# Kernel tuning notes

Measured on AMD Instinct MI355X. Metric: run time of the kernel, lower is better.

## Reference

```python
import jax, jax.numpy as jnp
import numpy as np
from jax import lax

B, DIM, H, W = 8, 128, 64, 64
CQ, DI, DS, RK = 32, 64, 16, 2  # quarter dim, d_inner=2*CQ, d_state, dt_rank=ceil(32/16)
EPS = 1e-5


def _dw(x, w, dil):
    # depthwise conv, x: [B,C,H,W], w: [C,1,kh,kw], torch padding='same'
    return lax.conv_general_dilated(x, w, (1, 1), 'SAME', rhs_dilation=(dil, dil),
                                    dimension_numbers=('NCHW', 'OIHW', 'NCHW'),
                                    feature_group_count=x.shape[1])


def _ln(x, g, b):
    mu = jnp.mean(x, -1, keepdims=True)
    v = jnp.mean((x - mu) ** 2, -1, keepdims=True)
    return (x - mu) * lax.rsqrt(v + EPS) * g + b


def _bn_eval(x, g, b):
    # BatchNorm2d eval mode with default running stats (mean 0, var 1)
    return x * lax.rsqrt(jnp.float32(1.0) + EPS) * g[None, :, None, None] + b[None, :, None, None]


def _axial_dw(x, kh, kw, k3, g, b, dil):
    y = _dw(x, kw, dil)   # (1,w) mixer
    y = _dw(y, kh, dil)   # (h,1) mixer
    y = _dw(y, k3, dil)   # 3x3 dw
    return _bn_eval(y, g, b) + x


def _vss(x, ln_g, ln_b, in_w, conv_w, conv_b, xproj_w, dtw, dtb, A_logs, Ds, on_g, on_b, out_w):
    # x: [B,H,W,CQ] channels-last; VMamba VSSBlock: x + SS2D(LN(x))
    Bb, Hh, Ww, _ = x.shape
    L = Hh * Ww
    xz = _ln(x, ln_g, ln_b) @ in_w.T                      # [B,H,W,2*DI]
    xw, z = jnp.split(xz, 2, axis=-1)
    xc = jax.nn.silu(_dw(xw.transpose(0, 3, 1, 2), conv_w, 1) + conv_b[None, :, None, None])
    xf = xc.reshape(Bb, DI, L)                            # row-major scan
    xwh = xc.transpose(0, 1, 3, 2).reshape(Bb, DI, L)     # column-major scan
    xs = jnp.stack([xf, xwh, jnp.flip(xf, -1), jnp.flip(xwh, -1)], axis=1)  # [B,4,DI,L]
    x_dbl = jnp.einsum('bkdl,kcd->bkcl', xs, xproj_w)     # [B,4,RK+2*DS,L]
    delta = jax.nn.softplus(jnp.einsum('bkrl,kdr->bkdl', x_dbl[:, :, :RK], dtw) + dtb[None, :, :, None])
    Bs, Cs = x_dbl[:, :, RK:RK + DS], x_dbl[:, :, RK + DS:]
    A = -jnp.exp(A_logs)                                  # [4,DI,DS]

    def step(h, t):
        u, d, Bt, Ct = t                                  # u,d:[B,4,DI]; Bt,Ct:[B,4,DS]
        h = h * jnp.exp(d[..., None] * A) + (d * u)[..., None] * Bt[:, :, None, :]
        return h, jnp.einsum('bkdn,bkn->bkd', h, Ct)

    seq = (xs.transpose(3, 0, 1, 2), delta.transpose(3, 0, 1, 2),
           Bs.transpose(3, 0, 1, 2), Cs.transpose(3, 0, 1, 2))
    _, ys = lax.scan(step, jnp.zeros((Bb, 4, DI, DS), x.dtype), seq)  # [L,B,4,DI]
    ys = ys.transpose(1, 2, 3, 0) + Ds[None, :, :, None] * xs         # [B,4,DI,L]
    y = ys[:, 0] + jnp.flip(ys[:, 2], -1)
    y_wh = ys[:, 1] + jnp.flip(ys[:, 3], -1)
    y = y + y_wh.reshape(Bb, DI, Ww, Hh).transpose(0, 1, 3, 2).reshape(Bb, DI, L)
    y = _ln(y.reshape(Bb, DI, Hh, Ww).transpose(0, 2, 3, 1), on_g, on_b)
    return x + (y * jax.nn.silu(z)) @ out_w.T


def _forward(x, dw1_kh, dw1_kw, dw1_k3, dw1_g, dw1_b, dw2_kh, dw2_kw, dw2_k3, dw2_g, dw2_b,
             dw3_kh, dw3_kw, dw3_k3, dw3_g, dw3_b, ln_g, ln_b, in_w, conv_w, conv_b, xproj_w,
             dtw, dtb, A_logs, Ds, on_g, on_b, out_w, scale1, scale2, scale3, scale4, bn_g, bn_b):
    x1, x2, x3, x4 = jnp.split(x, 4, axis=1)
    vp = (ln_g, ln_b, in_w, conv_w, conv_b, xproj_w, dtw, dtb, A_logs, Ds, on_g, on_b, out_w)

    def branch(xi, kh, kw, k3, g, b, dil, s):
        y = _axial_dw(xi, kh, kw, k3, g, b, dil)
        y = _vss(y.transpose(0, 2, 3, 1), *vp).transpose(0, 3, 1, 2)
        return y * s

    y1 = branch(x1, dw1_kh, dw1_kw, dw1_k3, dw1_g, dw1_b, 1, scale1)
    y2 = branch(x2, dw2_kh, dw2_kw, dw2_k3, dw2_g, dw2_b, 2, scale2)
    y3 = branch(x3, dw3_kh, dw3_kw, dw3_k3, dw3_g, dw3_b, 3, scale3)
    y4 = x4 * scale4
    return jax.nn.relu(_bn_eval(jnp.concatenate([y1, y2, y3, y4], 1), bn_g, bn_b))


def setup_inputs():
    ks = jax.random.split(jax.random.key(0), 40)
    rn = lambda k, s, sc: jax.random.normal(k, s, jnp.float32) * sc
    inp = {'x': jax.random.normal(ks[0], (B, DIM, H, W), jnp.float32)}
    for i, n in enumerate(['dw1', 'dw2', 'dw3']):
        inp[n + '_kh'] = rn(ks[1 + 3 * i], (CQ, 1, 7, 1), 0.2)
        inp[n + '_kw'] = rn(ks[2 + 3 * i], (CQ, 1, 1, 7), 0.2)
        inp[n + '_k3'] = rn(ks[3 + 3 * i], (CQ, 1, 3, 3), 0.2)
        inp[n + '_g'] = jnp.ones((CQ,))
        inp[n + '_b'] = jnp.zeros((CQ,))
    inp['ln_g'] = jnp.ones((CQ,))
    inp['ln_b'] = jnp.zeros((CQ,))
    inp['in_w'] = rn(ks[10], (2 * DI, CQ), 0.1)
    inp['conv_w'] = rn(ks[11], (DI, 1, 3, 3), 0.2)
    inp['conv_b'] = jnp.zeros((DI,))
    inp['xproj_w'] = rn(ks[12], (4, RK + 2 * DS, DI), 0.1)
    inp['dtw'] = rn(ks[13], (4, DI, RK), 0.5)
    inp['dtb'] = rn(ks[14], (4, DI), 0.5)
    inp['A_logs'] = jnp.log(jnp.broadcast_to(jnp.arange(1, DS + 1, dtype=jnp.float32), (4, DI, DS)))
    inp['Ds'] = jnp.ones((4, DI))
    inp['on_g'] = jnp.ones((DI,))
    inp['on_b'] = jnp.zeros((DI,))
    inp['out_w'] = rn(ks[15], (CQ, DI), 0.1)
    for n in ['scale1', 'scale2', 'scale3', 'scale4']:
        inp[n] = jnp.ones((1,))
    inp['bn_g'] = jnp.ones((DIM,))
    inp['bn_b'] = jnp.zeros((DIM,))
    return inp


def reference(x, dw1_kh, dw1_kw, dw1_k3, dw1_g, dw1_b, dw2_kh, dw2_kw, dw2_k3, dw2_g, dw2_b,
              dw3_kh, dw3_kw, dw3_k3, dw3_g, dw3_b, ln_g, ln_b, in_w, conv_w, conv_b, xproj_w,
              dtw, dtb, A_logs, Ds, on_g, on_b, out_w, scale1, scale2, scale3, scale4, bn_g, bn_b):
    return _forward(x, dw1_kh, dw1_kw, dw1_k3, dw1_g, dw1_b, dw2_kh, dw2_kw, dw2_k3, dw2_g, dw2_b,
                    dw3_kh, dw3_kw, dw3_k3, dw3_g, dw3_b, ln_g, ln_b, in_w, conv_w, conv_b, xproj_w,
                    dtw, dtb, A_logs, Ds, on_g, on_b, out_w, scale1, scale2, scale3, scale4, bn_g, bn_b)
```

## Files before the change

kernel.cpp:

```cpp
#include <hip/hip_runtime.h>
#include <hip/hip_bf16.h>
#include <cstdint>

typedef unsigned short ushort_t;
typedef float f32x2 __attribute__((ext_vector_type(2)));

__device__ __forceinline__ float softplus2(float x){
    return fmaxf(x, 0.f) + __logf(1.f + __expf(-fabsf(x)));
}
__device__ __forceinline__ float siluf(float x){
    return x / (1.f + __expf(-x));
}
__device__ __forceinline__ float b2f(ushort_t u){
    union { uint32_t i; float f; } v; v.i = ((uint32_t)u)<<16; return v.f;
}
__device__ __forceinline__ ushort_t f2b(float f){
    uint32_t x = __float_as_uint(f);
    uint32_t r = (x + 0x7FFFu + ((x>>16)&1u)) >> 16;
    return (ushort_t)r;
}

struct AxialParams {
    const float* kh[3]; const float* kw[3]; const float* k3[3];
    const float* g[3];  const float* b[3];
};

__global__ __launch_bounds__(256) void k_axial(const float* __restrict__ x,
                                               float* __restrict__ Y0, AxialParams P){
    __shared__ float s0[4096];
    __shared__ float s1[4096];
    int bid = blockIdx.x;
    int i = bid >> 8;
    int rem = bid & 255;
    int b = rem >> 5, c = rem & 31;
    int dil = i + 1;
    const float* xin = x + ((size_t)(b*128 + i*32 + c))*4096;
    float wkw[7], wkh[7], wk3[9];
    #pragma unroll
    for(int t=0;t<7;t++){ wkw[t]=P.kw[i][c*7+t]; wkh[t]=P.kh[i][c*7+t]; }
    #pragma unroll
    for(int t=0;t<9;t++) wk3[t]=P.k3[i][c*9+t];
    float gc = P.g[i][c], bc = P.b[i][c];
    int tid = threadIdx.x;
    for(int idx=tid; idx<4096; idx+=256) s0[idx]=xin[idx];
    __syncthreads();
    for(int idx=tid; idx<4096; idx+=256){
        int h=idx>>6, w=idx&63; float a=0.f;
        #pragma unroll
        for(int t=0;t<7;t++){ int ww=w+(t-3)*dil; if(ww>=0&&ww<64) a=fmaf(s0[h*64+ww],wkw[t],a); }
        s1[idx]=a;
    }
    __syncthreads();
    for(int idx=tid; idx<4096; idx+=256){
        int h=idx>>6, w=idx&63; float a=0.f;
        #pragma unroll
        for(int t=0;t<7;t++){ int hh=h+(t-3)*dil; if(hh>=0&&hh<64) a=fmaf(s1[hh*64+w],wkh[t],a); }
        s0[idx]=a;
    }
    __syncthreads();
    const float inv = rsqrtf(1.00001f);
    float* out = Y0 + ((size_t)(i*8+b)*32 + c)*4096;
    for(int idx=tid; idx<4096; idx+=256){
        int h=idx>>6, w=idx&63; float a=0.f;
        #pragma unroll
        for(int t=0;t<9;t++){
            int hh=h+((t/3)-1)*dil, ww=w+((t%3)-1)*dil;
            if(hh>=0&&hh<64&&ww>=0&&ww<64) a=fmaf(s0[hh*64+ww],wk3[t],a);
        }
        out[idx] = a*inv*gc + bc + xin[idx];
    }
}

__global__ __launch_bounds__(256) void k_lnproj(const float* __restrict__ Y0,
        const float* __restrict__ ln_g, const float* __restrict__ ln_b,
        const float* __restrict__ in_w, ushort_t* __restrict__ XW, ushort_t* __restrict__ ZS){
    __shared__ float W[128*32];
    int tid=threadIdx.x;
    for(int idx=tid; idx<4096; idx+=256) W[idx]=in_w[idx];
    __syncthreads();
    int pg = blockIdx.x*256 + tid;
    int ib = pg>>12, p = pg&4095;
    const float* src = Y0 + (size_t)ib*32*4096;
    float t[32];
    float mu=0.f;
    #pragma unroll
    for(int c=0;c<32;c++){ t[c]=src[c*4096+p]; mu+=t[c]; }
    mu *= (1.f/32.f);
    float v=0.f;
    #pragma unroll
    for(int c=0;c<32;c++){ float d=t[c]-mu; v+=d*d; }
    v *= (1.f/32.f);
    float rs = rsqrtf(v+1e-5f);
    #pragma unroll
    for(int c=0;c<32;c++) t[c] = (t[c]-mu)*rs*ln_g[c] + ln_b[c];
    ushort_t* xw = XW + (size_t)ib*64*4096 + p;
    ushort_t* zs = ZS + (size_t)ib*64*4096 + p;
    for(int j=0;j<64;j++){
        float a=0.f, a2=0.f;
        #pragma unroll
        for(int c=0;c<32;c++){
            a  = fmaf(t[c], W[j*32+c],      a);
            a2 = fmaf(t[c], W[(j+64)*32+c], a2);
        }
        xw[(size_t)j*4096] = f2b(a);
        zs[(size_t)j*4096] = f2b(siluf(a2));
    }
}

__global__ __launch_bounds__(256) void k_dwt(const ushort_t* __restrict__ XW,
        const float* __restrict__ cw, const float* __restrict__ cb,
        ushort_t* __restrict__ XC, ushort_t* __restrict__ XCT){
    __shared__ ushort_t sin_[4096];
    __shared__ ushort_t tr[64*66];
    int bid=blockIdx.x, tid=threadIdx.x;
    int d = bid&63;
    const ushort_t* src = XW + (size_t)bid*4096;
    for(int idx=tid; idx<1024; idx+=256)
        *reinterpret_cast<ushort4*>(&sin_[idx*4]) = *reinterpret_cast<const ushort4*>(&src[idx*4]);
    float wk[9];
    #pragma unroll
    for(int t=0;t<9;t++) wk[t]=cw[d*9+t];
    float bias=cb[d];
    __syncthreads();
    ushort_t* outp = XC + (size_t)bid*4096;
    for(int idx=tid; idx<4096; idx+=256){
        int h=idx>>6, wq=idx&63;
        float a=bias;
        #pragma unroll
        for(int t=0;t<9;t++){
            int hh=h+(t/3)-1, ww=wq+(t%3)-1;
            if(hh>=0&&hh<64&&ww>=0&&ww<64) a=fmaf(b2f(sin_[hh*64+ww]),wk[t],a);
        }
        ushort_t vb = f2b(siluf(a));
        outp[idx]=vb;
        tr[wq*66+h]=vb;
    }
    __syncthreads();
    ushort_t* outt = XCT + (size_t)bid*4096;
    for(int idx=tid; idx<4096; idx+=256){
        outt[idx]=tr[(idx>>6)*66+(idx&63)];
    }
}

__global__ __launch_bounds__(256) void k_transpose(const ushort_t* __restrict__ src, ushort_t* __restrict__ dst){
    __shared__ ushort_t tile[64*66];
    size_t plane = blockIdx.x;
    const ushort_t* s = src + plane*4096;
    ushort_t* d = dst + plane*4096;
    int tid=threadIdx.x;
    for(int idx=tid; idx<4096; idx+=256){
        int h=idx>>6, w=idx&63;
        tile[w*66+h]=s[idx];
    }
    __syncthreads();
    for(int idx=tid; idx<4096; idx+=256){
        d[idx]=tile[(idx>>6)*66 + (idx&63)];
    }
}

__global__ __launch_bounds__(256) void k_xdbl(const ushort_t* __restrict__ XC, const ushort_t* __restrict__ XCT,
        const float* __restrict__ xproj, ushort_t* __restrict__ XBb, ushort_t* __restrict__ XCc,
        float* __restrict__ DT){
    __shared__ float Wt[64][36];
    int bid=blockIdx.x; int tid=threadIdx.x;
    int ibk = bid>>4; int lb = bid&15;
    int k = ibk & 3; int ib = ibk>>2;
    for(int idx=tid; idx<2176; idx+=256){
        int c=idx>>6, dd=idx&63;
        Wt[dd][c]=xproj[k*2176+idx];
    }
    __syncthreads();
    int l = lb*256+tid;
    const ushort_t* src = ((k&1)?XCT:XC) + (size_t)ib*64*4096;
    int idxl = (k&2)? (4095-l) : l;
    float acc[34];
    #pragma unroll
    for(int c=0;c<34;c++) acc[c]=0.f;
    for(int dd=0;dd<64;dd++){
        float u = b2f(src[(size_t)dd*4096 + idxl]);
        float wv[36];
        const float4* wp = reinterpret_cast<const float4*>(&Wt[dd][0]);
        *reinterpret_cast<float4*>(&wv[0])  = wp[0];
        *reinterpret_cast<float4*>(&wv[4])  = wp[1];
        *reinterpret_cast<float4*>(&wv[8])  = wp[2];
        *reinterpret_cast<float4*>(&wv[12]) = wp[3];
        *reinterpret_cast<float4*>(&wv[16]) = wp[4];
        *reinterpret_cast<float4*>(&wv[20]) = wp[5];
        *reinterpret_cast<float4*>(&wv[24]) = wp[6];
        *reinterpret_cast<float4*>(&wv[28]) = wp[7];
        *reinterpret_cast<float2*>(&wv[32]) = *reinterpret_cast<const float2*>(&Wt[dd][32]);
        #pragma unroll
        for(int c=0;c<34;c++) acc[c] = fmaf(u, wv[c], acc[c]);
    }
    DT[((size_t)ibk*2)*4096 + l]   = acc[0];
    DT[((size_t)ibk*2+1)*4096 + l] = acc[1];
    ushort_t* ob = XBb + ((size_t)ibk*16)*4096 + l;
    ushort_t* oc = XCc + ((size_t)ibk*16)*4096 + l;
    #pragma unroll
    for(int c=0;c<16;c++){
        ob[(size_t)c*4096]=f2b(acc[2+c]);
        oc[(size_t)c*4096]=f2b(acc[18+c]);
    }
}


template<bool UNI>
__device__ __forceinline__ void scan1_body(int w,int d,float dt0,float dt1,float db,
    const float* An, f32x2* h2, float& S,
    const float (*sB)[64][16], const float (*sdt)[64][2], const ushort_t (*su)[66])
{
    for(int s=0;s<64;s++){
        const float* dp=&sdt[w][s][0];
        float delta=softplus2(fmaf(dt0,dp[0],fmaf(dt1,dp[1],db)));
        S+=delta;
        int j = w? 63-s : s;
        float du = delta*b2f(su[j][d]);
        float bb[16];
        const float4* bp=reinterpret_cast<const float4*>(&sB[w][s][0]);
        reinterpret_cast<float4*>(bb)[0]=bp[0];
        reinterpret_cast<float4*>(bb)[1]=bp[1];
        reinterpret_cast<float4*>(bb)[2]=bp[2];
        reinterpret_cast<float4*>(bb)[3]=bp[3];
        if(UNI){
            float r1=__expf(delta*An[0]);
            f32x2 a={r1,r1*r1}, rq={r1*r1,r1*r1}, du2={du,du};
            const f32x2* b2p=reinterpret_cast<const f32x2*>(bb);
            #pragma unroll
            for(int i=0;i<8;i++){ h2[i]=h2[i]*a+du2*b2p[i]; a=a*rq; }
        } else {
            float* hf=reinterpret_cast<float*>(h2);
            #pragma unroll
            for(int n=0;n<16;n++){ float a=__expf(delta*An[n]); hf[n]=fmaf(hf[n],a,du*bb[n]); }
        }
    }
}

__global__ __launch_bounds__(128) void k_scan1(const ushort_t* __restrict__ XBb, const float* __restrict__ DT,
        const ushort_t* __restrict__ XC, const ushort_t* __restrict__ XCT,
        const float* __restrict__ dtw, const float* __restrict__ dtb,
        const float* __restrict__ A_logs,
        ushort_t* __restrict__ CHS, float* __restrict__ SD){
    __shared__ float sB[2][64][16];
    __shared__ float sdt[2][64][2];
    __shared__ ushort_t su[64][66];
    int bid=blockIdx.x, tid=threadIdx.x;
    int ib = bid>>7; int rem = bid&127; int p = rem>>6; int ch = rem&63;
    int w = tid>>6, d = tid&63;
    int l0 = ch*64, r0 = 4032 - l0;
    const ushort_t* B0 = XBb + (size_t)(4*ib+p)*16*4096;
    const ushort_t* B1 = XBb + (size_t)(4*ib+p+2)*16*4096;
    for(int idx=tid; idx<512; idx+=128){
        int w2=idx>>8, n=(idx>>4)&15, q=(idx&15)*4;
        const ushort_t* Bs = w2? B1 : B0;
        int base = (w2? r0 : l0) + q;
        ushort4 v = *reinterpret_cast<const ushort4*>(&Bs[(size_t)n*4096 + base]);
        sB[w2][q+0][n]=b2f(v.x); sB[w2][q+1][n]=b2f(v.y); sB[w2][q+2][n]=b2f(v.z); sB[w2][q+3][n]=b2f(v.w);
    }
    {
        const float* D0 = DT + (size_t)(4*ib+p)*2*4096;
        const float* D1 = DT + (size_t)(4*ib+p+2)*2*4096;
        int r=tid>>6, s=tid&63;
        sdt[0][s][r] = D0[(size_t)r*4096 + l0 + s];
        sdt[1][s][r] = D1[(size_t)r*4096 + r0 + s];
    }
    const ushort_t* U = (p?XCT:XC) + (size_t)ib*64*4096;
    for(int idx=tid; idx<1024; idx+=128){
        int r=idx>>4, q=(idx&15)*4;
        ushort4 v = *reinterpret_cast<const ushort4*>(&U[(size_t)r*4096 + l0 + q]);
        su[q+0][r]=v.x; su[q+1][r]=v.y; su[q+2][r]=v.z; su[q+3][r]=v.w;
    }
    __syncthreads();
    int k = p + 2*w;
    float dt0=dtw[(k*64+d)*2], dt1=dtw[(k*64+d)*2+1], db=dtb[k*64+d];
    float An[16];
    #pragma unroll
    for(int n=0;n<16;n++) An[n] = -__expf(A_logs[(k*64+d)*16+n]);
    bool st = true;
    #pragma unroll
    for(int n=1;n<16;n++) st = st && (fabsf(An[n]-(n+1)*An[0]) <= 1e-4f*fabsf(An[n]) + 1e-6f);
    bool uni = (bool)__all((int)st);
    f32x2 h2[8];
    #pragma unroll
    for(int i=0;i<8;i++){ h2[i].x=0.f; h2[i].y=0.f; }
    float S=0.f;
    if(uni) scan1_body<true >(w,d,dt0,dt1,db,An,h2,S,sB,sdt,su);
    else    scan1_body<false>(w,d,dt0,dt1,db,An,h2,S,sB,sdt,su);
    int chd = w ? 63-ch : ch;
    ushort_t* o = CHS + ((size_t)(4*ib+k)*64 + chd)*1024 + d*16;
    const float* hf = reinterpret_cast<const float*>(h2);
    #pragma unroll
    for(int n=0;n<16;n++) o[n]=f2b(hf[n]);
    SD[((size_t)(4*ib+k)*64 + chd)*64 + d]=S;
}

__global__ __launch_bounds__(1024) void k_scan2(const float* __restrict__ A_logs,
        const float* __restrict__ SD, ushort_t* __restrict__ CHS){
    __shared__ float sS[4096];
    int ibk=blockIdx.x; int tid=threadIdx.x;
    for(int idx=tid; idx<4096; idx+=1024) sS[idx]=SD[(size_t)ibk*4096+idx];
    __syncthreads();
    int d=tid>>4, n=tid&15, k=ibk&3;
    float An = -__expf(A_logs[(k*64+d)*16+n]);
    float H=0.f;
    for(int c=0;c<64;c++){
        float pc = __expf(An*sS[c*64+d]);
        size_t o = ((size_t)ibk*64+c)*1024 + tid;
        float loc = b2f(CHS[o]);
        CHS[o]=f2b(H);
        H = fmaf(H, pc, loc);
    }
}

__device__ __forceinline__ const ushort_t* seg_src(int idx, int seg,
        const ushort_t* B0, const ushort_t* B1, const ushort_t* C0, const ushort_t* C1,
        int l0, int r0){
    int arr=idx>>8, w2=(idx>>7)&1, n=(idx>>3)&15, qi=idx&7;
    const ushort_t* S = arr? (w2?C1:C0) : (w2?B1:B0);
    int base = (w2? r0 : l0) + seg*32 + qi*4;
    return &S[(size_t)n*4096 + base];
}
__device__ __forceinline__ void seg_wr(int idx, ushort4 v,
        float (*sB)[32][16], float (*sC)[32][16]){
    int arr=idx>>8, w2=(idx>>7)&1, n=(idx>>3)&15, qi=idx&7;
    float (*dst)[32][16] = arr? sC : sB;
    int sl=qi*4;
    dst[w2][sl+0][n]=b2f(v.x); dst[w2][sl+1][n]=b2f(v.y);
    dst[w2][sl+2][n]=b2f(v.z); dst[w2][sl+3][n]=b2f(v.w);
}

template<bool UNI, int SEG>
__device__ __forceinline__ void scan3_seg(int w,int d,float dt0,float dt1,float db,
    const float* An, f32x2* h2,
    const float (*sB)[32][16], const float (*sC)[32][16],
    const float (*sdt)[64][2], const ushort_t (*su)[66], ushort_t (*sy)[66])
{
    for(int t=0;t<32;t++){
        int s = SEG*32 + t;
        const float* dp=&sdt[w][s][0];
        float delta=softplus2(fmaf(dt0,dp[0],fmaf(dt1,dp[1],db)));
        int j = w? 63-s : s;
        float du = delta*b2f(su[j][d]);
        float bb[16], cc[16];
        const float4* bp=reinterpret_cast<const float4*>(&sB[w][t][0]);
        const float4* cp=reinterpret_cast<const float4*>(&sC[w][t][0]);
        reinterpret_cast<float4*>(bb)[0]=bp[0]; reinterpret_cast<float4*>(bb)[1]=bp[1];
        reinterpret_cast<float4*>(bb)[2]=bp[2]; reinterpret_cast<float4*>(bb)[3]=bp[3];
        reinterpret_cast<float4*>(cc)[0]=cp[0]; reinterpret_cast<float4*>(cc)[1]=cp[1];
        reinterpret_cast<float4*>(cc)[2]=cp[2]; reinterpret_cast<float4*>(cc)[3]=cp[3];
        float y;
        if(UNI){
            float r1=__expf(delta*An[0]);
            f32x2 a={r1,r1*r1}, rq={r1*r1,r1*r1}, du2={du,du};
            f32x2 y2={0.f,0.f};
            const f32x2* b2p=reinterpret_cast<const f32x2*>(bb);
            const f32x2* c2p=reinterpret_cast<const f32x2*>(cc);
            #pragma unroll
            for(int i=0;i<8;i++){
                h2[i]=h2[i]*a+du2*b2p[i];
                y2=y2+h2[i]*c2p[i];
                a=a*rq;
            }
            y = y2.x + y2.y;
        } else {
            y=0.f;
            float* hf=reinterpret_cast<float*>(h2);
            #pragma unroll
            for(int n=0;n<16;n++){
                float a=__expf(delta*An[n]);
                hf[n]=fmaf(hf[n],a,du*bb[n]);
                y=fmaf(hf[n],cc[n],y);
            }
        }
        if(SEG==0) sy[j][d]=f2b(y);
        else       sy[j][d]=f2b(b2f(sy[j][d])+y);
    }
}

__global__ __launch_bounds__(128) void k_scan3(const ushort_t* __restrict__ XBb, const ushort_t* __restrict__ XCc,
        const float* __restrict__ DT,
        const ushort_t* __restrict__ XC, const ushort_t* __restrict__ XCT,
        const float* __restrict__ dtw, const float* __restrict__ dtb,
        const float* __restrict__ A_logs,
        const ushort_t* __restrict__ CHS,
        ushort_t* __restrict__ Y1, ushort_t* __restrict__ Y2){
    __shared__ float sB[2][32][16];
    __shared__ float sC[2][32][16];
    __shared__ float sdt[2][64][2];
    __shared__ ushort_t su[64][66];
    __shared__ ushort_t sy[64][66];
    int bid=blockIdx.x, tid=threadIdx.x;
    int ib = bid>>7; int rem = bid&127; int p = rem>>6; int ch = rem&63;
    int w = tid>>6, d = tid&63;
    int l0 = ch*64, r0 = 4032 - l0;
    const ushort_t* B0 = XBb + (size_t)(4*ib+p)*16*4096;
    const ushort_t* B1 = XBb + (size_t)(4*ib+p+2)*16*4096;
    const ushort_t* C0 = XCc + (size_t)(4*ib+p)*16*4096;
    const ushort_t* C1 = XCc + (size_t)(4*ib+p+2)*16*4096;
    for(int idx=tid; idx<512; idx+=128)
        seg_wr(idx, *reinterpret_cast<const ushort4*>(seg_src(idx,0,B0,B1,C0,C1,l0,r0)), sB, sC);
    {
        const float* D0 = DT + (size_t)(4*ib+p)*2*4096;
        const float* D1 = DT + (size_t)(4*ib+p+2)*2*4096;
        int r=tid>>6, s=tid&63;
        sdt[0][s][r] = D0[(size_t)r*4096 + l0 + s];
        sdt[1][s][r] = D1[(size_t)r*4096 + r0 + s];
    }
    const ushort_t* U = (p?XCT:XC) + (size_t)ib*64*4096;
    for(int idx=tid; idx<1024; idx+=128){
        int r=idx>>4, q=(idx&15)*4;
        ushort4 v = *reinterpret_cast<const ushort4*>(&U[(size_t)r*4096 + l0 + q]);
        su[q+0][r]=v.x; su[q+1][r]=v.y; su[q+2][r]=v.z; su[q+3][r]=v.w;
    }
    __syncthreads();
    ushort4 pf[4];
    #pragma unroll
    for(int r=0;r<4;r++)
        pf[r] = *reinterpret_cast<const ushort4*>(seg_src(tid+r*128,1,B0,B1,C0,C1,l0,r0));
    int k = p + 2*w;
    float dt0=dtw[(k*64+d)*2], dt1=dtw[(k*64+d)*2+1], db=dtb[k*64+d];
    float An[16];
    #pragma unroll
    for(int n=0;n<16;n++) An[n] = -__expf(A_logs[(k*64+d)*16+n]);
    bool st = true;
    #pragma unroll
    for(int n=1;n<16;n++) st = st && (fabsf(An[n]-(n+1)*An[0]) <= 1e-4f*fabsf(An[n]) + 1e-6f);
    bool uni = (bool)__all((int)st);
    int chd = w ? 63-ch : ch;
    const ushort_t* e = CHS + ((size_t)(4*ib+k)*64 + chd)*1024 + d*16;
    f32x2 h2[8];
    {
        float* hf = reinterpret_cast<float*>(h2);
        #pragma unroll
        for(int n=0;n<16;n++) hf[n]=b2f(e[n]);
    }
    if(uni) scan3_seg<true ,0>(w,d,dt0,dt1,db,An,h2,sB,sC,sdt,su,sy);
    else    scan3_seg<false,0>(w,d,dt0,dt1,db,An,h2,sB,sC,sdt,su,sy);
    __syncthreads();
    #pragma unroll
    for(int r=0;r<4;r++) seg_wr(tid+r*128, pf[r], sB, sC);
    __syncthreads();
    if(uni) scan3_seg<true ,1>(w,d,dt0,dt1,db,An,h2,sB,sC,sdt,su,sy);
    else    scan3_seg<false,1>(w,d,dt0,dt1,db,An,h2,sB,sC,sdt,su,sy);
    __syncthreads();
    ushort_t* Yb = (p?Y2:Y1) + (size_t)ib*64*4096;
    for(int idx=tid; idx<1024; idx+=128){
        int r=idx>>4, q=(idx&15)*4;
        ushort4 v;
        v.x=sy[q+0][r]; v.y=sy[q+1][r]; v.z=sy[q+2][r]; v.w=sy[q+3][r];
        *reinterpret_cast<ushort4*>(&Yb[(size_t)r*4096 + l0 + q]) = v;
    }
}

__global__ __launch_bounds__(256) void k_final(const ushort_t* __restrict__ Y1, const ushort_t* __restrict__ Y2T,
        const ushort_t* __restrict__ ZS, const float* __restrict__ Y0,
        const ushort_t* __restrict__ XC, const float* __restrict__ Ds,
        const float* __restrict__ on_g, const float* __restrict__ on_b,
        const float* __restrict__ out_w,
        const float* __restrict__ s1, const float* __restrict__ s2, const float* __restrict__ s3,
        const float* __restrict__ bn_g, const float* __restrict__ bn_b,
        float* __restrict__ out){
    __shared__ float W[32*64];
    __shared__ float sD[64];
    int tid=threadIdx.x;
    for(int idx=tid; idx<2048; idx+=256) W[idx]=out_w[idx];
    if(tid<64) sD[tid]=Ds[tid]+Ds[64+tid]+Ds[128+tid]+Ds[192+tid];
    __syncthreads();
    int pg=blockIdx.x*256+tid;
    int ib=pg>>12, p=pg&4095;
    int i=ib>>3, b=ib&7;
    float y[64];
    const ushort_t* y1 = Y1 + (size_t)ib*64*4096 + p;
    const ushort_t* y2 = Y2T + (size_t)ib*64*4096 + p;
    const ushort_t* xc = XC + (size_t)ib*64*4096 + p;
    float mu=0.f;
    #pragma unroll
    for(int dd=0;dd<64;dd++){
        y[dd]=b2f(y1[(size_t)dd*4096])+b2f(y2[(size_t)dd*4096])+sD[dd]*b2f(xc[(size_t)dd*4096]);
        mu+=y[dd];
    }
    mu*=(1.f/64.f);
    float v=0.f;
    #pragma unroll
    for(int dd=0;dd<64;dd++){ float q=y[dd]-mu; v+=q*q; }
    v*=(1.f/64.f);
    float rs=rsqrtf(v+1e-5f);
    const ushort_t* zs = ZS + (size_t)ib*64*4096 + p;
    #pragma unroll
    for(int dd=0;dd<64;dd++){
        float yn=(y[dd]-mu)*rs*on_g[dd]+on_b[dd];
        y[dd]=yn*b2f(zs[(size_t)dd*4096]);
    }
    float sc = (i==0)?s1[0]:((i==1)?s2[0]:s3[0]);
    const float inv = rsqrtf(1.00001f);
    const float* y0 = Y0 + (size_t)ib*32*4096 + p;
    for(int c=0;c<32;c++){
        float a=0.f;
        #pragma unroll
        for(int dd=0;dd<64;dd++) a=fmaf(y[dd],W[c*64+dd],a);
        float o=(y0[(size_t)c*4096]+a)*sc;
        int chn=i*32+c;
        float vv=fmaf(o*inv, bn_g[chn], bn_b[chn]);
        out[((size_t)b*128+chn)*4096 + p]=fmaxf(vv,0.f);
    }
}

__global__ __launch_bounds__(256) void k_branch4(const float* __restrict__ x,
        const float* __restrict__ s4, const float* __restrict__ bn_g,
        const float* __restrict__ bn_b, float* __restrict__ out){
    int g=blockIdx.x*256+threadIdx.x;
    int b=g>>17; int rem=g&131071; int c=rem>>12; int p=rem&4095;
    int chn=96+c;
    const float inv=rsqrtf(1.00001f);
    float v=x[((size_t)b*128+chn)*4096+p]*s4[0];
    v=fmaf(v*inv, bn_g[chn], bn_b[chn]);
    out[((size_t)b*128+chn)*4096+p]=fmaxf(v,0.f);
}

extern "C" void kernel_launch(void* const* d_in, const int* in_sizes, int n_in,
                              void* d_out, int out_size, void* d_ws, size_t ws_size,
                              hipStream_t stream) {
    const float* x      = (const float*)d_in[0];
    const float* ln_g   = (const float*)d_in[16];
    const float* ln_b   = (const float*)d_in[17];
    const float* in_w   = (const float*)d_in[18];
    const float* conv_w = (const float*)d_in[19];
    const float* conv_b = (const float*)d_in[20];
    const float* xproj  = (const float*)d_in[21];
    const float* dtw    = (const float*)d_in[22];
    const float* dtb    = (const float*)d_in[23];
    const float* A_logs = (const float*)d_in[24];
    const float* Ds     = (const float*)d_in[25];
    const float* on_g   = (const float*)d_in[26];
    const float* on_b   = (const float*)d_in[27];
    const float* out_w  = (const float*)d_in[28];
    const float* sc1    = (const float*)d_in[29];
    const float* sc2    = (const float*)d_in[30];
    const float* sc3    = (const float*)d_in[31];
    const float* sc4    = (const float*)d_in[32];
    const float* bn_g   = (const float*)d_in[33];
    const float* bn_b   = (const float*)d_in[34];

    AxialParams P;
    for(int i=0;i<3;i++){
        P.kh[i]=(const float*)d_in[1+5*i];
        P.kw[i]=(const float*)d_in[2+5*i];
        P.k3[i]=(const float*)d_in[3+5*i];
        P.g[i] =(const float*)d_in[4+5*i];
        P.b[i] =(const float*)d_in[5+5*i];
    }

    char* base = (char*)d_ws;
    float*    Y0   = (float*)   (base + 0);
    ushort_t* ZS   = (ushort_t*)(base + 12582912);
    ushort_t* XC   = (ushort_t*)(base + 25165824);
    ushort_t* XCT  = (ushort_t*)(base + 37748736);
    ushort_t* XBb  = (ushort_t*)(base + 50331648);
    ushort_t* XW   = (ushort_t*)(base + 50331648);
    ushort_t* XCc  = (ushort_t*)(base + 62914560);
    float*    DT   = (float*)   (base + 75497472);
    ushort_t* CHS  = (ushort_t*)(base + 78643200);
    float*    SD   = (float*)   (base + 91226112);
    ushort_t* Y1   = (ushort_t*)(base + 92798976);
    ushort_t* Y2   = (ushort_t*)(base + 105381888);
    ushort_t* Y2T  = XBb;

    float* out = (float*)d_out;

    k_axial    <<<768,   256, 0, stream>>>(x, Y0, P);
    k_lnproj   <<<384,   256, 0, stream>>>(Y0, ln_g, ln_b, in_w, XW, ZS);
    k_dwt      <<<1536,  256, 0, stream>>>(XW, conv_w, conv_b, XC, XCT);
    k_xdbl     <<<1536,  256, 0, stream>>>(XC, XCT, xproj, XBb, XCc, DT);
    k_scan1    <<<3072,  128, 0, stream>>>(XBb, DT, XC, XCT, dtw, dtb, A_logs, CHS, SD);
    k_scan2    <<<96,   1024, 0, stream>>>(A_logs, SD, CHS);
    k_scan3    <<<3072,  128, 0, stream>>>(XBb, XCc, DT, XC, XCT, dtw, dtb, A_logs, CHS, Y1, Y2);
    k_transpose<<<1536,  256, 0, stream>>>(Y2, Y2T);
    k_final    <<<384,   256, 0, stream>>>(Y1, Y2T, ZS, Y0, XC, Ds, on_g, on_b, out_w,
                                           sc1, sc2, sc3, bn_g, bn_b, out);
    k_branch4  <<<4096,  256, 0, stream>>>(x, sc4, bn_g, bn_b, out);
}
```

Baseline: 286.6 us.

## Restructure scan output layout, share xdbl input tile, double-buffer scan1 B loads

k_xdbl now stages one 128-position input tile in shared memory and reuses it for both the forward and flipped directions, so each XC/XCT element is read once instead of twice. k_scan1 loads B in two 32-step segments and prefetches the second segment into registers while the first is scanned. When the workspace is large enough, k_scan3 writes each direction's output directly into a per-position, channel-contiguous YS buffer. A new k_finalA then sums the four directions with vector loads, which removes the shared-memory staging, the separate transpose kernel and the Y1/Y2 round trip. This adds a workspace-size-dependent code path, and its per-thread YS writes are strided by 64 elements (128 bytes) per position, which may coalesce poorly.

```diff
diff --git a/kernel.cpp b/kernel.cpp
--- a/kernel.cpp
+++ b/kernel.cpp
@@ -19,6 +19,8 @@
     uint32_t r = (x + 0x7FFFu + ((x>>16)&1u)) >> 16;
     return (ushort_t)r;
 }
+__device__ __forceinline__ float lo16(uint32_t u){ return __uint_as_float(u<<16); }
+__device__ __forceinline__ float hi16(uint32_t u){ return __uint_as_float(u & 0xffff0000u); }
 
 struct AxialParams {
     const float* kh[3]; const float* kw[3]; const float* k3[3];
@@ -158,65 +160,106 @@
     }
 }
 
-__global__ __launch_bounds__(256) void k_xdbl(const ushort_t* __restrict__ XC, const ushort_t* __restrict__ XCT,
+__global__ __launch_bounds__(128) void k_xdbl(const ushort_t* __restrict__ XC, const ushort_t* __restrict__ XCT,
         const float* __restrict__ xproj, ushort_t* __restrict__ XBb, ushort_t* __restrict__ XCc,
         float* __restrict__ DT){
+    __shared__ ushort_t tile[64][128];
     __shared__ float Wt[64][36];
-    int bid=blockIdx.x; int tid=threadIdx.x;
-    int ibk = bid>>4; int lb = bid&15;
-    int k = ibk & 3; int ib = ibk>>2;
-    for(int idx=tid; idx<2176; idx+=256){
-        int c=idx>>6, dd=idx&63;
-        Wt[dd][c]=xproj[k*2176+idx];
-    }
-    __syncthreads();
-    int l = lb*256+tid;
-    const ushort_t* src = ((k&1)?XCT:XC) + (size_t)ib*64*4096;
-    int idxl = (k&2)? (4095-l) : l;
-    float acc[34];
-    #pragma unroll
-    for(int c=0;c<34;c++) acc[c]=0.f;
-    for(int dd=0;dd<64;dd++){
-        float u = b2f(src[(size_t)dd*4096 + idxl]);
-        float wv[36];
-        const float4* wp = reinterpret_cast<const float4*>(&Wt[dd][0]);
-        *reinterpret_cast<float4*>(&wv[0])  = wp[0];
-        *reinterpret_cast<float4*>(&wv[4])  = wp[1];
-        *reinterpret_cast<float4*>(&wv[8])  = wp[2];
-        *reinterpret_cast<float4*>(&wv[12]) = wp[3];
-        *reinterpret_cast<float4*>(&wv[16]) = wp[4];
-        *reinterpret_cast<float4*>(&wv[20]) = wp[5];
-        *reinterpret_cast<float4*>(&wv[24]) = wp[6];
-        *reinterpret_cast<float4*>(&wv[28]) = wp[7];
-        *reinterpret_cast<float2*>(&wv[32]) = *reinterpret_cast<const float2*>(&Wt[dd][32]);
-        #pragma unroll
-        for(int c=0;c<34;c++) acc[c] = fmaf(u, wv[c], acc[c]);
-    }
-    DT[((size_t)ibk*2)*4096 + l]   = acc[0];
-    DT[((size_t)ibk*2+1)*4096 + l] = acc[1];
-    ushort_t* ob = XBb + ((size_t)ibk*16)*4096 + l;
-    ushort_t* oc = XCc + ((size_t)ibk*16)*4096 + l;
-    #pragma unroll
-    for(int c=0;c<16;c++){
-        ob[(size_t)c*4096]=f2b(acc[2+c]);
-        oc[(size_t)c*4096]=f2b(acc[18+c]);
-    }
-}
-
+    int bid=blockIdx.x, tid=threadIdx.x;
+    int lb = bid&31, t=(bid>>5)&1, ib=bid>>6;
+    int m0 = lb*128;
+    const ushort_t* src = (t?XCT:XC) + (size_t)ib*64*4096;
+    for(int idx=tid; idx<2048; idx+=128){
+        int dd=idx>>5, q=(idx&31)*4;
+        *reinterpret_cast<ushort4*>(&tile[dd][q]) =
+            *reinterpret_cast<const ushort4*>(&src[(size_t)dd*4096 + m0 + q]);
+    }
+    int m = m0 + tid;
+    for(int pass=0; pass<2; ++pass){
+        int k = t + 2*pass;
+        __syncthreads();
+        for(int idx=tid; idx<2176; idx+=128){
+            int c=idx>>6, dd=idx&63;
+            Wt[dd][c]=xproj[k*2176+idx];
+        }
+        __syncthreads();
+        float acc[34];
+        #pragma unroll
+        for(int c=0;c<34;c++) acc[c]=0.f;
+        for(int dd=0;dd<64;dd++){
+            float u = b2f(tile[dd][tid]);
+            float wv[36];
+            const float4* wp = reinterpret_cast<const float4*>(&Wt[dd][0]);
+            *reinterpret_cast<float4*>(&wv[0])  = wp[0];
+            *reinterpret_cast<float4*>(&wv[4])  = wp[1];
+            *reinterpret_cast<float4*>(&wv[8])  = wp[2];
+            *reinterpret_cast<float4*>(&wv[12]) = wp[3];
+            *reinterpret_cast<float4*>(&wv[16]) = wp[4];
+            *reinterpret_cast<float4*>(&wv[20]) = wp[5];
+            *reinterpret_cast<float4*>(&wv[24]) = wp[6];
+            *reinterpret_cast<float4*>(&wv[28]) = wp[7];
+            *reinterpret_cast<float2*>(&wv[32]) = *reinterpret_cast<const float2*>(&Wt[dd][32]);
+            #pragma unroll
+            for(int c=0;c<34;c++) acc[c] = fmaf(u, wv[c], acc[c]);
+        }
+        int l = pass ? (4095-m) : m;
+        DT[((size_t)(ib*4+k)*2)*4096 + l]   = acc[0];
+        DT[((size_t)(ib*4+k)*2+1)*4096 + l] = acc[1];
+        ushort_t* ob = XBb + ((size_t)(ib*4+k)*16)*4096 + l;
+        ushort_t* oc = XCc + ((size_t)(ib*4+k)*16)*4096 + l;
+        #pragma unroll
+        for(int c=0;c<16;c++){
+            ob[(size_t)c*4096]=f2b(acc[2+c]);
+            oc[(size_t)c*4096]=f2b(acc[18+c]);
+        }
+    }
+}
+
+
+__device__ __forceinline__ const ushort_t* b_src(int idx, int seg,
+        const ushort_t* B0, const ushort_t* B1, int l0, int r0){
+    int n=idx&15, qi=(idx>>4)&7, w2=idx>>7;
+    const ushort_t* S = w2?B1:B0;
+    int base = (w2? r0 : l0) + seg*32 + qi*4;
+    return &S[(size_t)n*4096 + base];
+}
+__device__ __forceinline__ void b_wr(int idx, ushort4 v, float (*sB)[32][16]){
+    int n=idx&15, qi=(idx>>4)&7, w2=idx>>7;
+    int sl=qi*4;
+    sB[w2][sl+0][n]=b2f(v.x); sB[w2][sl+1][n]=b2f(v.y);
+    sB[w2][sl+2][n]=b2f(v.z); sB[w2][sl+3][n]=b2f(v.w);
+}
+__device__ __forceinline__ const ushort_t* bc_src(int idx, int seg,
+        const ushort_t* B0, const ushort_t* B1, const ushort_t* C0, const ushort_t* C1,
+        int l0, int r0){
+    int n=idx&15, qi=(idx>>4)&7, w2=(idx>>7)&1, arr=idx>>8;
+    const ushort_t* S = arr? (w2?C1:C0) : (w2?B1:B0);
+    int base = (w2? r0 : l0) + seg*32 + qi*4;
+    return &S[(size_t)n*4096 + base];
+}
+__device__ __forceinline__ void bc_wr(int idx, ushort4 v,
+        float (*sB)[32][16], float (*sC)[32][16]){
+    int n=idx&15, qi=(idx>>4)&7, w2=(idx>>7)&1, arr=idx>>8;
+    float (*dst)[32][16] = arr? sC : sB;
+    int sl=qi*4;
+    dst[w2][sl+0][n]=b2f(v.x); dst[w2][sl+1][n]=b2f(v.y);
+    dst[w2][sl+2][n]=b2f(v.z); dst[w2][sl+3][n]=b2f(v.w);
+}
 
 template<bool UNI>
-__device__ __forceinline__ void scan1_body(int w,int d,float dt0,float dt1,float db,
-    const float* An, f32x2* h2, float& S,
-    const float (*sB)[64][16], const float (*sdt)[64][2], const ushort_t (*su)[66])
+__device__ __forceinline__ void scan1_seg(int w,int d,float dt0,float dt1,float db,
+    const float* An, f32x2* h2, float& S, int S0,
+    const float (*sB)[32][16], const float (*sdt)[64][2], const ushort_t (*su)[66])
 {
-    for(int s=0;s<64;s++){
+    for(int t=0;t<32;t++){
+        int s = S0 + t;
         const float* dp=&sdt[w][s][0];
         float delta=softplus2(fmaf(dt0,dp[0],fmaf(dt1,dp[1],db)));
         S+=delta;
         int j = w? 63-s : s;
         float du = delta*b2f(su[j][d]);
         float bb[16];
-        const float4* bp=reinterpret_cast<const float4*>(&sB[w][s][0]);
+        const float4* bp=reinterpret_cast<const float4*>(&sB[w][t][0]);
         reinterpret_cast<float4*>(bb)[0]=bp[0];
         reinterpret_cast<float4*>(bb)[1]=bp[1];
         reinterpret_cast<float4*>(bb)[2]=bp[2];
@@ -240,7 +283,7 @@
         const float* __restrict__ dtw, const float* __restrict__ dtb,
         const float* __restrict__ A_logs,
         ushort_t* __restrict__ CHS, float* __restrict__ SD){
-    __shared__ float sB[2][64][16];
+    __shared__ float sB[2][32][16];
     __shared__ float sdt[2][64][2];
     __shared__ ushort_t su[64][66];
     int bid=blockIdx.x, tid=threadIdx.x;
@@ -249,13 +292,8 @@
     int l0 = ch*64, r0 = 4032 - l0;
     const ushort_t* B0 = XBb + (size_t)(4*ib+p)*16*4096;
     const ushort_t* B1 = XBb + (size_t)(4*ib+p+2)*16*4096;
-    for(int idx=tid; idx<512; idx+=128){
-        int w2=idx>>8, n=(idx>>4)&15, q=(idx&15)*4;
-        const ushort_t* Bs = w2? B1 : B0;
-        int base = (w2? r0 : l0) + q;
-        ushort4 v = *reinterpret_cast<const ushort4*>(&Bs[(size_t)n*4096 + base]);
-        sB[w2][q+0][n]=b2f(v.x); sB[w2][q+1][n]=b2f(v.y); sB[w2][q+2][n]=b2f(v.z); sB[w2][q+3][n]=b2f(v.w);
-    }
+    for(int idx=tid; idx<256; idx+=128)
+        b_wr(idx, *reinterpret_cast<const ushort4*>(b_src(idx,0,B0,B1,l0,r0)), sB);
     {
         const float* D0 = DT + (size_t)(4*ib+p)*2*4096;
         const float* D1 = DT + (size_t)(4*ib+p+2)*2*4096;
@@ -270,6 +308,10 @@
         su[q+0][r]=v.x; su[q+1][r]=v.y; su[q+2][r]=v.z; su[q+3][r]=v.w;
     }
     __syncthreads();
+    ushort4 pf[2];
+    #pragma unroll
+    for(int r=0;r<2;r++)
+        pf[r] = *reinterpret_cast<const ushort4*>(b_src(tid+r*128,1,B0,B1,l0,r0));
     int k = p + 2*w;
     float dt0=dtw[(k*64+d)*2], dt1=dtw[(k*64+d)*2+1], db=dtb[k*64+d];
     float An[16];
@@ -283,8 +325,14 @@
     #pragma unroll
     for(int i=0;i<8;i++){ h2[i].x=0.f; h2[i].y=0.f; }
     float S=0.f;
-    if(uni) scan1_body<true >(w,d,dt0,dt1,db,An,h2,S,sB,sdt,su);
-    else    scan1_body<false>(w,d,dt0,dt1,db,An,h2,S,sB,sdt,su);
+    if(uni) scan1_seg<true >(w,d,dt0,dt1,db,An,h2,S,0,sB,sdt,su);
+    else    scan1_seg<false>(w,d,dt0,dt1,db,An,h2,S,0,sB,sdt,su);
+    __syncthreads();
+    #pragma unroll
+    for(int r=0;r<2;r++) b_wr(tid+r*128, pf[r], sB);
+    __syncthreads();
+    if(uni) scan1_seg<true >(w,d,dt0,dt1,db,An,h2,S,32,sB,sdt,su);
+    else    scan1_seg<false>(w,d,dt0,dt1,db,An,h2,S,32,sB,sdt,su);
     int chd = w ? 63-ch : ch;
     ushort_t* o = CHS + ((size_t)(4*ib+k)*64 + chd)*1024 + d*16;
     const float* hf = reinterpret_cast<const float*>(h2);
@@ -311,28 +359,12 @@
     }
 }
 
-__device__ __forceinline__ const ushort_t* seg_src(int idx, int seg,
-        const ushort_t* B0, const ushort_t* B1, const ushort_t* C0, const ushort_t* C1,
-        int l0, int r0){
-    int arr=idx>>8, w2=(idx>>7)&1, n=(idx>>3)&15, qi=idx&7;
-    const ushort_t* S = arr? (w2?C1:C0) : (w2?B1:B0);
-    int base = (w2? r0 : l0) + seg*32 + qi*4;
-    return &S[(size_t)n*4096 + base];
-}
-__device__ __forceinline__ void seg_wr(int idx, ushort4 v,
-        float (*sB)[32][16], float (*sC)[32][16]){
-    int arr=idx>>8, w2=(idx>>7)&1, n=(idx>>3)&15, qi=idx&7;
-    float (*dst)[32][16] = arr? sC : sB;
-    int sl=qi*4;
-    dst[w2][sl+0][n]=b2f(v.x); dst[w2][sl+1][n]=b2f(v.y);
-    dst[w2][sl+2][n]=b2f(v.z); dst[w2][sl+3][n]=b2f(v.w);
-}
-
-template<bool UNI, int SEG>
+template<bool UNI, int SEG, int MODE>
 __device__ __forceinline__ void scan3_seg(int w,int d,float dt0,float dt1,float db,
     const float* An, f32x2* h2,
     const float (*sB)[32][16], const float (*sC)[32][16],
-    const float (*sdt)[64][2], const ushort_t (*su)[66], ushort_t (*sy)[66])
+    const float (*sdt)[64][2], const ushort_t (*su)[66],
+    ushort_t (*sy)[66], ushort_t* ysrow)
 {
     for(int t=0;t<32;t++){
         int s = SEG*32 + t;
@@ -371,23 +403,28 @@
                 y=fmaf(hf[n],cc[n],y);
             }
         }
-        if(SEG==0) sy[j][d]=f2b(y);
-        else       sy[j][d]=f2b(b2f(sy[j][d])+y);
-    }
-}
-
+        if(MODE==1){
+            ysrow[(size_t)j<<6] = f2b(y);
+        } else {
+            if(SEG==0) sy[j][d]=f2b(y);
+            else       sy[j][d]=f2b(b2f(sy[j][d])+y);
+        }
+    }
+}
+
+template<int MODE>
 __global__ __launch_bounds__(128) void k_scan3(const ushort_t* __restrict__ XBb, const ushort_t* __restrict__ XCc,
         const float* __restrict__ DT,
         const ushort_t* __restrict__ XC, const ushort_t* __restrict__ XCT,
         const float* __restrict__ dtw, const float* __restrict__ dtb,
         const float* __restrict__ A_logs,
         const ushort_t* __restrict__ CHS,
-        ushort_t* __restrict__ Y1, ushort_t* __restrict__ Y2){
+        ushort_t* __restrict__ Y1, ushort_t* __restrict__ Y2, ushort_t* __restrict__ YS){
     __shared__ float sB[2][32][16];
     __shared__ float sC[2][32][16];
     __shared__ float sdt[2][64][2];
     __shared__ ushort_t su[64][66];
-    __shared__ ushort_t sy[64][66];
+    __shared__ ushort_t sy[(MODE==0)?64:1][66];
     int bid=blockIdx.x, tid=threadIdx.x;
     int ib = bid>>7; int rem = bid&127; int p = rem>>6; int ch = rem&63;
     int w = tid>>6, d = tid&63;
@@ -397,7 +434,7 @@
     const ushort_t* C0 = XCc + (size_t)(4*ib+p)*16*4096;
     const ushort_t* C1 = XCc + (size_t)(4*ib+p+2)*16*4096;
     for(int idx=tid; idx<512; idx+=128)
-        seg_wr(idx, *reinterpret_cast<const ushort4*>(seg_src(idx,0,B0,B1,C0,C1,l0,r0)), sB, sC);
+        bc_wr(idx, *reinterpret_cast<const ushort4*>(bc_src(idx,0,B0,B1,C0,C1,l0,r0)), sB, sC);
     {
         const float* D0 = DT + (size_t)(4*ib+p)*2*4096;
         const float* D1 = DT + (size_t)(4*ib+p+2)*2*4096;
@@ -415,7 +452,7 @@
     ushort4 pf[4];
     #pragma unroll
     for(int r=0;r<4;r++)
-        pf[r] = *reinterpret_cast<const ushort4*>(seg_src(tid+r*128,1,B0,B1,C0,C1,l0,r0));
+        pf[r] = *reinterpret_cast<const ushort4*>(bc_src(tid+r*128,1,B0,B1,C0,C1,l0,r0));
     int k = p + 2*w;
     float dt0=dtw[(k*64+d)*2], dt1=dtw[(k*64+d)*2+1], db=dtb[k*64+d];
     float An[16];
@@ -433,21 +470,26 @@
         #pragma unroll
         for(int n=0;n<16;n++) hf[n]=b2f(e[n]);
     }
-    if(uni) scan3_seg<true ,0>(w,d,dt0,dt1,db,An,h2,sB,sC,sdt,su,sy);
-    else    scan3_seg<false,0>(w,d,dt0,dt1,db,An,h2,sB,sC,sdt,su,sy);
-    __syncthreads();
-    #pragma unroll
-    for(int r=0;r<4;r++) seg_wr(tid+r*128, pf[r], sB, sC);
-    __syncthreads();
-    if(uni) scan3_seg<true ,1>(w,d,dt0,dt1,db,An,h2,sB,sC,sdt,su,sy);
-    else    scan3_seg<false,1>(w,d,dt0,dt1,db,An,h2,sB,sC,sdt,su,sy);
-    __syncthreads();
-    ushort_t* Yb = (p?Y2:Y1) + (size_t)ib*64*4096;
-    for(int idx=tid; idx<1024; idx+=128){
-        int r=idx>>4, q=(idx&15)*4;
-        ushort4 v;
-        v.x=sy[q+0][r]; v.y=sy[q+1][r]; v.z=sy[q+2][r]; v.w=sy[q+3][r];
-        *reinterpret_cast<ushort4*>(&Yb[(size_t)r*4096 + l0 + q]) = v;
+    ushort_t* ysrow = nullptr;
+    if constexpr(MODE==1)
+        ysrow = YS + ((size_t)(4*ib+k)*4096 + l0)*64 + d;
+    if(uni) scan3_seg<true ,0,MODE>(w,d,dt0,dt1,db,An,h2,sB,sC,sdt,su,sy,ysrow);
+    else    scan3_seg<false,0,MODE>(w,d,dt0,dt1,db,An,h2,sB,sC,sdt,su,sy,ysrow);
+    __syncthreads();
+    #pragma unroll
+    for(int r=0;r<4;r++) bc_wr(tid+r*128, pf[r], sB, sC);
+    __syncthreads();
+    if(uni) scan3_seg<true ,1,MODE>(w,d,dt0,dt1,db,An,h2,sB,sC,sdt,su,sy,ysrow);
+    else    scan3_seg<false,1,MODE>(w,d,dt0,dt1,db,An,h2,sB,sC,sdt,su,sy,ysrow);
+    if constexpr(MODE==0){
+        __syncthreads();
+        ushort_t* Yb = (p?Y2:Y1) + (size_t)ib*64*4096;
+        for(int idx=tid; idx<1024; idx+=128){
+            int r=idx>>4, q=(idx&15)*4;
+            ushort4 v;
+            v.x=sy[q+0][r]; v.y=sy[q+1][r]; v.z=sy[q+2][r]; v.w=sy[q+3][r];
+            *reinterpret_cast<ushort4*>(&Yb[(size_t)r*4096 + l0 + q]) = v;
+        }
     }
 }
 
@@ -477,6 +519,74 @@
     for(int dd=0;dd<64;dd++){
         y[dd]=b2f(y1[(size_t)dd*4096])+b2f(y2[(size_t)dd*4096])+sD[dd]*b2f(xc[(size_t)dd*4096]);
         mu+=y[dd];
+    }
+    mu*=(1.f/64.f);
+    float v=0.f;
+    #pragma unroll
+    for(int dd=0;dd<64;dd++){ float q=y[dd]-mu; v+=q*q; }
+    v*=(1.f/64.f);
+    float rs=rsqrtf(v+1e-5f);
+    const ushort_t* zs = ZS + (size_t)ib*64*4096 + p;
+    #pragma unroll
+    for(int dd=0;dd<64;dd++){
+        float yn=(y[dd]-mu)*rs*on_g[dd]+on_b[dd];
+        y[dd]=yn*b2f(zs[(size_t)dd*4096]);
+    }
+    float sc = (i==0)?s1[0]:((i==1)?s2[0]:s3[0]);
+    const float inv = rsqrtf(1.00001f);
+    const float* y0 = Y0 + (size_t)ib*32*4096 + p;
+    for(int c=0;c<32;c++){
+        float a=0.f;
+        #pragma unroll
+        for(int dd=0;dd<64;dd++) a=fmaf(y[dd],W[c*64+dd],a);
+        float o=(y0[(size_t)c*4096]+a)*sc;
+        int chn=i*32+c;
+        float vv=fmaf(o*inv, bn_g[chn], bn_b[chn]);
+        out[((size_t)b*128+chn)*4096 + p]=fmaxf(vv,0.f);
+    }
+}
+
+__global__ __launch_bounds__(256) void k_finalA(const ushort_t* __restrict__ YS,
+        const ushort_t* __restrict__ ZS, const float* __restrict__ Y0,
+        const ushort_t* __restrict__ XC, const float* __restrict__ Ds,
+        const float* __restrict__ on_g, const float* __restrict__ on_b,
+        const float* __restrict__ out_w,
+        const float* __restrict__ s1, const float* __restrict__ s2, const float* __restrict__ s3,
+        const float* __restrict__ bn_g, const float* __restrict__ bn_b,
+        float* __restrict__ out){
+    __shared__ float W[32*64];
+    __shared__ float sD[64];
+    int tid=threadIdx.x;
+    for(int idx=tid; idx<2048; idx+=256) W[idx]=out_w[idx];
+    if(tid<64) sD[tid]=Ds[tid]+Ds[64+tid]+Ds[128+tid]+Ds[192+tid];
+    __syncthreads();
+    int pg=blockIdx.x*256+tid;
+    int ib=pg>>12, p=pg&4095;
+    int i=ib>>3, b=ib&7;
+    int lt = ((p&63)<<6) | (p>>6);
+    const uint4* q0 = reinterpret_cast<const uint4*>(YS + ((size_t)(ib*4+0)*4096 + p )*64);
+    const uint4* q1 = reinterpret_cast<const uint4*>(YS + ((size_t)(ib*4+1)*4096 + lt)*64);
+    const uint4* q2 = reinterpret_cast<const uint4*>(YS + ((size_t)(ib*4+2)*4096 + p )*64);
+    const uint4* q3 = reinterpret_cast<const uint4*>(YS + ((size_t)(ib*4+3)*4096 + lt)*64);
+    const ushort_t* xc = XC + (size_t)ib*64*4096 + p;
+    float y[64];
+    float mu=0.f;
+    #pragma unroll
+    for(int qq=0; qq<8; ++qq){
+        uint4 a0=q0[qq], a1=q1[qq], a2=q2[qq], a3=q3[qq];
+        const uint32_t* u0=reinterpret_cast<const uint32_t*>(&a0);
+        const uint32_t* u1=reinterpret_cast<const uint32_t*>(&a1);
+        const uint32_t* u2=reinterpret_cast<const uint32_t*>(&a2);
+        const uint32_t* u3=reinterpret_cast<const uint32_t*>(&a3);
+        #pragma unroll
+        for(int e=0;e<4;e++){
+            int dd = qq*8 + e*2;
+            float ylo = lo16(u0[e])+lo16(u1[e])+lo16(u2[e])+lo16(u3[e]);
+            float yhi = hi16(u0[e])+hi16(u1[e])+hi16(u2[e])+hi16(u3[e]);
+            y[dd]   = ylo + sD[dd]  *b2f(xc[(size_t)dd*4096]);
+            y[dd+1] = yhi + sD[dd+1]*b2f(xc[(size_t)(dd+1)*4096]);
+            mu += y[dd] + y[dd+1];
+        }
     }
     mu*=(1.f/64.f);
     float v=0.f;
@@ -560,21 +670,32 @@
     float*    DT   = (float*)   (base + 75497472);
     ushort_t* CHS  = (ushort_t*)(base + 78643200);
     float*    SD   = (float*)   (base + 91226112);
+    ushort_t* YS   = (ushort_t*)(base + 92798976);
     ushort_t* Y1   = (ushort_t*)(base + 92798976);
     ushort_t* Y2   = (ushort_t*)(base + 105381888);
     ushort_t* Y2T  = XBb;
 
+    bool primary = (ws_size >= 143130624ull);
+
     float* out = (float*)d_out;
 
     k_axial    <<<768,   256, 0, stream>>>(x, Y0, P);
     k_lnproj   <<<384,   256, 0, stream>>>(Y0, ln_g, ln_b, in_w, XW, ZS);
     k_dwt      <<<1536,  256, 0, stream>>>(XW, conv_w, conv_b, XC, XCT);
-    k_xdbl     <<<1536,  256, 0, stream>>>(XC, XCT, xproj, XBb, XCc, DT);
+    k_xdbl     <<<1536,  128, 0, stream>>>(XC, XCT, xproj, XBb, XCc, DT);
     k_scan1    <<<3072,  128, 0, stream>>>(XBb, DT, XC, XCT, dtw, dtb, A_logs, CHS, SD);
     k_scan2    <<<96,   1024, 0, stream>>>(A_logs, SD, CHS);
-    k_scan3    <<<3072,  128, 0, stream>>>(XBb, XCc, DT, XC, XCT, dtw, dtb, A_logs, CHS, Y1, Y2);
-    k_transpose<<<1536,  256, 0, stream>>>(Y2, Y2T);
-    k_final    <<<384,   256, 0, stream>>>(Y1, Y2T, ZS, Y0, XC, Ds, on_g, on_b, out_w,
-                                           sc1, sc2, sc3, bn_g, bn_b, out);
+    if(primary){
+        k_scan3<1> <<<3072, 128, 0, stream>>>(XBb, XCc, DT, XC, XCT, dtw, dtb, A_logs, CHS,
+                                              nullptr, nullptr, YS);
+        k_finalA   <<<384,  256, 0, stream>>>(YS, ZS, Y0, XC, Ds, on_g, on_b, out_w,
+                                              sc1, sc2, sc3, bn_g, bn_b, out);
+    } else {
+        k_scan3<0> <<<3072, 128, 0, stream>>>(XBb, XCc, DT, XC, XCT, dtw, dtb, A_logs, CHS,
+                                              Y1, Y2, nullptr);
+        k_transpose<<<1536, 256, 0, stream>>>(Y2, Y2T);
+        k_final    <<<384,  256, 0, stream>>>(Y1, Y2T, ZS, Y0, XC, Ds, on_g, on_b, out_w,
+                                              sc1, sc2, sc3, bn_g, bn_b, out);
+    }
     k_branch4  <<<4096,  256, 0, stream>>>(x, sc4, bn_g, bn_b, out);
 }
```

New measurement: 326.3 us. +13.8%, slower.
